# Kernel tuning notes

Hardware: AMD Instinct MI355X
Metric: run time of the kernel (lower is better)

The kernel has to match this reference:

```python
import jax, jax.numpy as jnp
import numpy as np

EPS = 1e-6
NEG = -10000.0
B, T, V, D, H, L, F = 2, 1024, 32000, 1024, 16, 4, 2730
DH = D // H
SCALE = 1.0 / np.sqrt(DH)


def alibi_slopes(n_head):
    # standard ALiBi geometric slopes (n_head is a power of 2 here)
    start = 2.0 ** (-8.0 / n_head)
    return jnp.asarray([start ** (i + 1) for i in range(n_head)], dtype=jnp.float32)


def rational_softmax(x, eps=EPS):
    # exp-free softmax: Pade [0/2] rational surrogate of exp on shifted (<=0) scores
    s = x - jnp.max(x, axis=-1, keepdims=True)
    num = 1.0 / (1.0 - s + 0.5 * s * s)
    return num / (jnp.sum(num, axis=-1, keepdims=True) + eps)


def me_norm(x, w, eps=EPS):
    # mean-error norm: x / (mean|x| + eps) * w
    return x / (jnp.mean(jnp.abs(x), axis=-1, keepdims=True) + eps) * w


def setup_inputs() -> dict:
    key = jax.random.key(0)
    ks = jax.random.split(key, 9)
    std = 0.02
    return {
        "input_ids": jax.random.randint(ks[0], (B, T), 0, V),
        "embed_w":   jax.random.normal(ks[1], (V, D), jnp.float32) * std,  # tied with head
        "qkv_w":     jax.random.normal(ks[2], (L, 3 * D, D), jnp.float32) * std,
        "out_w":     jax.random.normal(ks[3], (L, D, D), jnp.float32) * std,
        "gate_w":    jax.random.normal(ks[4], (L, 2 * F, D), jnp.float32) * std,
        "wout_w":    jax.random.normal(ks[5], (L, D, F), jnp.float32) * std,
        "norm1_w":   jnp.ones((L, D), jnp.float32),
        "norm2_w":   jnp.ones((L, D), jnp.float32),
        "normf_w":   jnp.ones((D,), jnp.float32),
    }


def _forward(input_ids, embed_w, qkv_w, out_w, gate_w, wout_w, norm1_w, norm2_w, normf_w):
    slopes = alibi_slopes(H)                       # [H]
    pos = jnp.arange(T)
    rel = jnp.abs(pos[:, None] - pos[None, :]).astype(jnp.float32)  # [T,T]
    alibi = -rel[None] * slopes[:, None, None]     # [H,T,T]
    causal = jnp.triu(jnp.ones((T, T), bool), k=1) # future positions

    x = embed_w[input_ids]                         # [B,T,D]

    def block(x, p):
        w_qkv, w_out, w_gate, w_wout, n1, n2 = p
        h = me_norm(x, n1)
        qkv = (h @ w_qkv.T).reshape(B, T, 3, H, DH).transpose(2, 0, 3, 1, 4)
        q, k, v = qkv[0], qkv[1], qkv[2]           # [B,H,T,DH]
        scores = jnp.einsum('bhtd,bhsd->bhts', q, k) * SCALE + alibi
        scores = jnp.where(causal[None, None], NEG, scores)
        probs = rational_softmax(scores)
        o = jnp.einsum('bhts,bhsd->bhtd', probs, v)
        o = o.transpose(0, 2, 1, 3).reshape(B, T, D)
        x = x + o @ w_out.T
        h = me_norm(x, n2)
        gv = h @ w_gate.T                           # [B,T,2F]
        gate, val = gv[..., :F], gv[..., F:]
        sigma = 0.5 * (gate / (jnp.abs(gate) + 1.0) + 1.0)  # rational sigmoid
        x = x + (gate * sigma * val) @ w_wout.T
        return x, None

    x, _ = jax.lax.scan(block, x, (qkv_w, out_w, gate_w, wout_w, norm1_w, norm2_w))
    x = me_norm(x, normf_w)
    logits = x @ embed_w.T                          # tied head, [B,T,V]
    return logits


def reference(input_ids, embed_w, qkv_w, out_w, gate_w, wout_w, norm1_w, norm2_w, normf_w):
    return _forward(input_ids, embed_w, qkv_w, out_w, gate_w, wout_w, norm1_w, norm2_w, normf_w)
```

## Files before the change

### kernel.cpp

```cpp
#include <hip/hip_runtime.h>
#include <math.h>

typedef __attribute__((ext_vector_type(8))) short bf16x8;
typedef __attribute__((ext_vector_type(4))) float f32x4;

namespace {
constexpr int Bc = 2, Tc = 1024, Dc = 1024, Hc = 16, Fc = 2730;
constexpr int Fp = 2752;
constexpr int Gp = 5504;
constexpr int Mc = Bc * Tc;
constexpr float EPSc = 1e-6f;
constexpr float NEGc = -10000.0f;
constexpr float SCALEc = 0.125f;
}

__device__ __forceinline__ unsigned short f2b(float f) {
    unsigned int u = __float_as_uint(f);
    u += 0x7FFFu + ((u >> 16) & 1u);
    return (unsigned short)(u >> 16);
}

__global__ void k_embed(const int* __restrict__ ids, const float* __restrict__ ew,
                        float* __restrict__ x) {
    int row = blockIdx.x;
    int id = ids[row];
    const float4* src = (const float4*)(ew + (size_t)id * Dc);
    float4* dst = (float4*)(x + (size_t)row * Dc);
    dst[threadIdx.x] = src[threadIdx.x];
}

__global__ void k_conv(const float* __restrict__ in, unsigned short* __restrict__ out) {
    size_t i = ((size_t)blockIdx.x * 256 + threadIdx.x) * 4;
    float4 v = *(const float4*)(in + i);
    ushort4 o;
    o.x = f2b(v.x); o.y = f2b(v.y); o.z = f2b(v.z); o.w = f2b(v.w);
    *(ushort4*)(out + i) = o;
}

__global__ void k_conv_gate_ilv(const float* __restrict__ in, unsigned short* __restrict__ out) {
    int r = blockIdx.x;
    int c = threadIdx.x * 4;
    ushort4 o;
    if (r < 2 * Fc) {
        int src = (r >> 1) + (r & 1) * Fc;
        float4 v = *(const float4*)(in + (size_t)src * Dc + c);
        o.x = f2b(v.x); o.y = f2b(v.y); o.z = f2b(v.z); o.w = f2b(v.w);
    } else {
        o.x = o.y = o.z = o.w = 0;
    }
    *(ushort4*)(out + (size_t)r * Dc + c) = o;
}

__global__ void k_conv_padk(const float* __restrict__ in, unsigned short* __restrict__ out) {
    int r = blockIdx.x;
    for (int c = threadIdx.x; c < Fp; c += 256) {
        float v = (c < Fc) ? in[(size_t)r * Fc + c] : 0.0f;
        out[(size_t)r * Fp + c] = f2b(v);
    }
}

__global__ void k_menorm_b(const float* __restrict__ x, const float* __restrict__ w,
                           unsigned short* __restrict__ out) {
    int row = blockIdx.x;
    float4 v = ((const float4*)(x + (size_t)row * Dc))[threadIdx.x];
    float s = fabsf(v.x) + fabsf(v.y) + fabsf(v.z) + fabsf(v.w);
#pragma unroll
    for (int m = 32; m >= 1; m >>= 1) s += __shfl_xor(s, m);
    __shared__ float ws4[4];
    if ((threadIdx.x & 63) == 0) ws4[threadIdx.x >> 6] = s;
    __syncthreads();
    float tot = ws4[0] + ws4[1] + ws4[2] + ws4[3];
    float inv = 1.0f / (tot / (float)Dc + EPSc);
    float4 wv = ((const float4*)w)[threadIdx.x];
    ushort4 o;
    o.x = f2b(v.x * inv * wv.x);
    o.y = f2b(v.y * inv * wv.y);
    o.z = f2b(v.z * inv * wv.z);
    o.w = f2b(v.w * inv * wv.w);
    ((ushort4*)(out + (size_t)row * Dc))[threadIdx.x] = o;
}

template <int MODE, int BM>
__global__ __launch_bounds__(256) void k_mfma_gemm(
    const unsigned short* __restrict__ A, const unsigned short* __restrict__ Bw,
    const float* __restrict__ Res, float* __restrict__ C,
    unsigned short* __restrict__ U0, unsigned short* __restrict__ U1,
    unsigned short* __restrict__ U2, int N, int K) {
    constexpr int MFR = BM / 32;
    __shared__ __align__(16) unsigned short As[BM * 64];
    __shared__ __align__(16) unsigned short Bs[128 * 64];
    const int tid = threadIdx.x;
    const int lane = tid & 63;
    const int wid = tid >> 6;
    const int wr = wid >> 1, wc = wid & 1;
    const int l15 = lane & 15, g = lane >> 4;

    const int nwg = gridDim.x * gridDim.y;
    int w = blockIdx.y * gridDim.x + blockIdx.x;
    int f = (nwg & 7) ? w : ((w & 7) * (nwg >> 3) + (w >> 3));
    const int bm = (f % gridDim.x) * BM, bn = (f / gridDim.x) * 128;

    f32x4 acc[MFR][4] = {};

    const int nk = K >> 6;
    for (int kt = 0; kt < nk; ++kt) {
        const int k0 = kt << 6;
#pragma unroll
        for (int it = 0; it < MFR; ++it) {
            int ci = it * 256 + tid;
            int r = ci >> 3;
            int sc = (ci & 7) ^ (r & 7);
            __builtin_amdgcn_global_load_lds(
                (const __attribute__((address_space(1))) void*)(A + (size_t)(bm + r) * K + k0 + sc * 8),
                (__attribute__((address_space(3))) void*)(As + ci * 8), 16, 0, 0);
        }
#pragma unroll
        for (int it = 0; it < 4; ++it) {
            int ci = it * 256 + tid;
            int r = ci >> 3;
            int sc = (ci & 7) ^ (r & 7);
            __builtin_amdgcn_global_load_lds(
                (const __attribute__((address_space(1))) void*)(Bw + (size_t)(bn + r) * K + k0 + sc * 8),
                (__attribute__((address_space(3))) void*)(Bs + ci * 8), 16, 0, 0);
        }
        __syncthreads();
#pragma unroll
        for (int kk = 0; kk < 2; ++kk) {
            bf16x8 af[MFR], bfr[4];
            const int kc = kk * 4 + g;
#pragma unroll
            for (int m = 0; m < MFR; ++m) {
                int row = wr * (BM / 2) + m * 16 + l15;
                af[m] = *(const bf16x8*)&As[(row * 8 + (kc ^ (row & 7))) * 8];
            }
#pragma unroll
            for (int n = 0; n < 4; ++n) {
                int col = wc * 64 + n * 16 + l15;
                bfr[n] = *(const bf16x8*)&Bs[(col * 8 + (kc ^ (col & 7))) * 8];
            }
#pragma unroll
            for (int m = 0; m < MFR; ++m)
#pragma unroll
                for (int n = 0; n < 4; ++n)
                    acc[m][n] = __builtin_amdgcn_mfma_f32_16x16x32_bf16(af[m], bfr[n], acc[m][n], 0, 0, 0);
        }
        __syncthreads();
    }

#pragma unroll
    for (int m = 0; m < MFR; ++m) {
        int row0 = bm + wr * (BM / 2) + m * 16 + (g << 2);
#pragma unroll
        for (int n = 0; n < 4; ++n) {
            int col = bn + wc * 64 + n * 16 + l15;
            if constexpr (MODE == 0 || MODE == 1) {
#pragma unroll
                for (int j = 0; j < 4; ++j) {
                    size_t idx = (size_t)(row0 + j) * N + col;
                    float v = acc[m][n][j];
                    if (MODE == 1) v += Res[idx];
                    C[idx] = v;
                }
            } else if constexpr (MODE == 2) {
                if (col < 2048) {
                    unsigned short* dst = (col < 1024) ? U0 : U1;
                    int hh = (col & 1023) >> 6, dh = col & 63;
#pragma unroll
                    for (int j = 0; j < 4; ++j) {
                        int row = row0 + j;
                        int b = row >> 10, t = row & 1023;
                        dst[((size_t)((b * Hc + hh) * Tc + t)) * 64 + dh] = f2b(acc[m][n][j]);
                    }
                } else {
                    int hh = (col >> 6) & 15, dh = col & 63;
                    int b = row0 >> 10, t = row0 & 1023;
                    ushort4 o4;
                    o4.x = f2b(acc[m][n][0]); o4.y = f2b(acc[m][n][1]);
                    o4.z = f2b(acc[m][n][2]); o4.w = f2b(acc[m][n][3]);
                    *(ushort4*)&U2[((size_t)((b * Hc + hh) * 64 + dh)) * Tc + t] = o4;
                }
            } else {
                float pv[4];
#pragma unroll
                for (int j = 0; j < 4; ++j) pv[j] = __shfl_xor(acc[m][n][j], 1);
                if ((l15 & 1) == 0) {
                    int fq = col >> 1;
#pragma unroll
                    for (int j = 0; j < 4; ++j) {
                        float gate = acc[m][n][j], val = pv[j];
                        float sigma = 0.5f * (gate / (fabsf(gate) + 1.0f) + 1.0f);
                        U0[(size_t)(row0 + j) * Fp + fq] = f2b(gate * sigma * val);
                    }
                }
            }
        }
    }
}

__global__ __launch_bounds__(256) void k_attn_mfma(
    const unsigned short* __restrict__ Qh, const unsigned short* __restrict__ Kh,
    const unsigned short* __restrict__ Vt, unsigned short* __restrict__ o) {
    const int q0 = blockIdx.x * 64;
    const int h = blockIdx.y, b = blockIdx.z;
    const int bh = b * Hc + h;
    const float slope = exp2f(-0.5f * (float)(h + 1));

    __shared__ __align__(16) unsigned short Ks[64 * 64];
    __shared__ __align__(16) unsigned short Vs[64 * 64];
    __shared__ __align__(16) unsigned short Ps[4][16 * 64];

    const int tid = threadIdx.x, lane = tid & 63, wid = tid >> 6;
    const int q0w = q0 + wid * 16;
    const int l15 = lane & 15, g = lane >> 4;

    const unsigned short* qbase = Qh + ((size_t)(bh * Tc + q0w + l15)) * 64 + g * 8;
    bf16x8 qf[2];
    qf[0] = *(const bf16x8*)qbase;
    qf[1] = *(const bf16x8*)(qbase + 32);

    const int nt = q0 / 64 + 1;

    f32x4 mx = {-3e38f, -3e38f, -3e38f, -3e38f};
    for (int it = 0; it < nt; ++it) {
        const int st = it * 64;
        __syncthreads();
#pragma unroll
        for (int half = 0; half < 2; ++half) {
            int ci = half * 256 + tid;
            int r = ci >> 3, sc = (ci & 7) ^ (r & 7);
            __builtin_amdgcn_global_load_lds(
                (const __attribute__((address_space(1))) void*)(Kh + ((size_t)(bh * Tc + st + r)) * 64 + sc * 8),
                (__attribute__((address_space(3))) void*)(Ks + ci * 8), 16, 0, 0);
        }
        __syncthreads();
#pragma unroll
        for (int si = 0; si < 4; ++si) {
            f32x4 d = {0.f, 0.f, 0.f, 0.f};
#pragma unroll
            for (int kc = 0; kc < 2; ++kc) {
                int r2 = si * 16 + l15;
                int c2 = kc * 4 + g;
                bf16x8 bk = *(const bf16x8*)&Ks[(r2 * 8 + (c2 ^ (r2 & 7))) * 8];
                d = __builtin_amdgcn_mfma_f32_16x16x32_bf16(qf[kc], bk, d, 0, 0, 0);
            }
            int s = st + si * 16 + l15;
#pragma unroll
            for (int j = 0; j < 4; ++j) {
                int t = q0w + g * 4 + j;
                float scv = (s <= t) ? d[j] * SCALEc - slope * (float)(t - s) : -3e38f;
                mx[j] = fmaxf(mx[j], scv);
            }
        }
    }
#pragma unroll
    for (int m = 8; m >= 1; m >>= 1)
#pragma unroll
        for (int j = 0; j < 4; ++j) mx[j] = fmaxf(mx[j], __shfl_xor(mx[j], m));

    f32x4 sum = {0.f, 0.f, 0.f, 0.f};
    f32x4 oacc[4] = {};
    for (int it = 0; it < nt; ++it) {
        const int st = it * 64;
        __syncthreads();
#pragma unroll
        for (int half = 0; half < 2; ++half) {
            int ci = half * 256 + tid;
            int r = ci >> 3, sc = (ci & 7) ^ (r & 7);
            __builtin_amdgcn_global_load_lds(
                (const __attribute__((address_space(1))) void*)(Kh + ((size_t)(bh * Tc + st + r)) * 64 + sc * 8),
                (__attribute__((address_space(3))) void*)(Ks + ci * 8), 16, 0, 0);
            __builtin_amdgcn_global_load_lds(
                (const __attribute__((address_space(1))) void*)(Vt + ((size_t)(bh * 64 + r)) * Tc + st + sc * 8),
                (__attribute__((address_space(3))) void*)(Vs + ci * 8), 16, 0, 0);
        }
        __syncthreads();
#pragma unroll
        for (int si = 0; si < 4; ++si) {
            f32x4 d = {0.f, 0.f, 0.f, 0.f};
#pragma unroll
            for (int kc = 0; kc < 2; ++kc) {
                int r2 = si * 16 + l15;
                int c2 = kc * 4 + g;
                bf16x8 bk = *(const bf16x8*)&Ks[(r2 * 8 + (c2 ^ (r2 & 7))) * 8];
                d = __builtin_amdgcn_mfma_f32_16x16x32_bf16(qf[kc], bk, d, 0, 0, 0);
            }
            int sl = si * 16 + l15;
            int s = st + sl;
            int chunk = sl >> 3, coff = sl & 7;
#pragma unroll
            for (int j = 0; j < 4; ++j) {
                int t = q0w + g * 4 + j;
                int q = g * 4 + j;
                unsigned short pb = 0;
                if (s <= t) {
                    float sv = d[j] * SCALEc - slope * (float)(t - s) - mx[j];
                    float num = __builtin_amdgcn_rcpf(fmaf(0.5f * sv, sv, 1.0f - sv));
                    sum[j] += num;
                    pb = f2b(num);
                }
                Ps[wid][q * 64 + ((chunk ^ (q & 7)) * 8) + coff] = pb;
            }
        }
        __syncthreads();
#pragma unroll
        for (int kc = 0; kc < 2; ++kc) {
            int c2 = kc * 4 + g;
            bf16x8 pa = *(const bf16x8*)&Ps[wid][(l15 * 8 + (c2 ^ (l15 & 7))) * 8];
#pragma unroll
            for (int n = 0; n < 4; ++n) {
                int r2 = n * 16 + l15;
                bf16x8 vb = *(const bf16x8*)&Vs[(r2 * 8 + (c2 ^ (r2 & 7))) * 8];
                oacc[n] = __builtin_amdgcn_mfma_f32_16x16x32_bf16(pa, vb, oacc[n], 0, 0, 0);
            }
        }
    }
#pragma unroll
    for (int m = 8; m >= 1; m >>= 1)
#pragma unroll
        for (int j = 0; j < 4; ++j) sum[j] += __shfl_xor(sum[j], m);

#pragma unroll
    for (int j = 0; j < 4; ++j) {
        int t = q0w + g * 4 + j;
        float svm = NEGc - mx[j];
        float mnum = __builtin_amdgcn_rcpf(fmaf(0.5f * svm, svm, 1.0f - svm));
        float inv = __builtin_amdgcn_rcpf(sum[j] + (float)(Tc - 1 - t) * mnum + EPSc);
#pragma unroll
        for (int n = 0; n < 4; ++n) {
            o[((size_t)(b * Tc + t)) * Dc + h * 64 + n * 16 + l15] = f2b(oacc[n][j] * inv);
        }
    }
}

extern "C" void kernel_launch(void* const* d_in, const int* in_sizes, int n_in,
                              void* d_out, int out_size, void* d_ws, size_t ws_size,
                              hipStream_t stream) {
    const int* ids = (const int*)d_in[0];
    const float* embed_w = (const float*)d_in[1];
    const float* qkv_w = (const float*)d_in[2];
    const float* out_w = (const float*)d_in[3];
    const float* gate_w = (const float*)d_in[4];
    const float* wout_w = (const float*)d_in[5];
    const float* n1 = (const float*)d_in[6];
    const float* n2 = (const float*)d_in[7];
    const float* nf = (const float*)d_in[8];
    float* outp = (float*)d_out;

    char* ws = (char*)d_ws;
    float* x = (float*)(ws + 0);
    unsigned short* h = (unsigned short*)(ws + 8388608);
    unsigned short* Qh = (unsigned short*)(ws + 12582912);
    unsigned short* Kh = (unsigned short*)(ws + 16777216);
    unsigned short* Vt = (unsigned short*)(ws + 20971520);
    unsigned short* g = (unsigned short*)(ws + 25165824);
    unsigned short* w1 = (unsigned short*)(ws + 36438016);
    unsigned short* wo_b = (unsigned short*)(ws + 42729472);
    unsigned short* wg_b = (unsigned short*)(ws + 44826624);
    unsigned short* emb_b = (unsigned short*)(ws + 12582912);

    dim3 blk(256);

    k_embed<<<dim3(Mc), blk, 0, stream>>>(ids, embed_w, x);

    for (int l = 0; l < 4; l++) {
        const float* wq = qkv_w + (size_t)l * 3 * Dc * Dc;
        const float* wo = out_w + (size_t)l * Dc * Dc;
        const float* wg = gate_w + (size_t)l * 2 * Fc * Dc;
        const float* ww = wout_w + (size_t)l * Dc * Fc;

        k_conv<<<dim3(3072), blk, 0, stream>>>(wq, w1);
        k_conv<<<dim3(1024), blk, 0, stream>>>(wo, wo_b);
        k_conv_gate_ilv<<<dim3(Gp), blk, 0, stream>>>(wg, wg_b);

        k_menorm_b<<<dim3(Mc), blk, 0, stream>>>(x, n1 + (size_t)l * Dc, h);
        k_mfma_gemm<2, 128><<<dim3(16, 24), blk, 0, stream>>>(h, w1, nullptr, nullptr, Qh, Kh, Vt, 3 * Dc, Dc);
        k_conv_padk<<<dim3(1024), blk, 0, stream>>>(ww, w1);
        k_attn_mfma<<<dim3(Tc / 64, Hc, Bc), blk, 0, stream>>>(Qh, Kh, Vt, h);
        k_mfma_gemm<1, 64><<<dim3(32, 8), blk, 0, stream>>>(h, wo_b, x, x, nullptr, nullptr, nullptr, Dc, Dc);
        k_menorm_b<<<dim3(Mc), blk, 0, stream>>>(x, n2 + (size_t)l * Dc, h);
        k_mfma_gemm<3, 128><<<dim3(16, Gp / 128), blk, 0, stream>>>(h, wg_b, nullptr, nullptr, g, nullptr, nullptr, Gp, Dc);
        k_mfma_gemm<1, 64><<<dim3(32, 8), blk, 0, stream>>>(g, w1, x, x, nullptr, nullptr, nullptr, Dc, Fp);
    }

    k_menorm_b<<<dim3(Mc), blk, 0, stream>>>(x, nf, h);
    k_conv<<<dim3(32000), blk, 0, stream>>>(embed_w, emb_b);
    k_mfma_gemm<0, 128><<<dim3(16, 250), blk, 0, stream>>>(h, emb_b, nullptr, outp, nullptr, nullptr, nullptr, 32000, Dc);
}
```

Before: 1.053 ms.

## Add 256x256 eight-wave pipelined GEMM for the tied LM head

Adds a 512-thread GEMM kernel for the final vocabulary projection. It uses 256x256 tiles, double-buffered direct global-to-LDS loads with an XOR swizzle, XCD-aware block remapping, and MFMA phases raised with s_setprio. It replaces the 128-tile generic GEMM for the largest matmul to get more reuse per loaded tile and to overlap loads with MFMA work. The cost is a large LDS footprint (128KB) and 128 accumulators per thread, which may limit occupancy. The grid is only 1000 blocks.

```diff
diff --git a/kernel.cpp b/kernel.cpp
--- a/kernel.cpp
+++ b/kernel.cpp
@@ -197,6 +197,114 @@
     }
 }
 
+__global__ __launch_bounds__(512, 2) void k_gemm_8ph(
+    const unsigned short* __restrict__ A, const unsigned short* __restrict__ Bw,
+    float* __restrict__ C, int N, int K) {
+    __shared__ __align__(16) unsigned short As[2][256 * 64];
+    __shared__ __align__(16) unsigned short Bs[2][256 * 64];
+    const int tid = threadIdx.x;
+    const int lane = tid & 63, wid = tid >> 6;
+    const int wm = wid >> 2, wn = wid & 3;
+    const int l15 = lane & 15, g = lane >> 4;
+
+    const int nwg = gridDim.x * gridDim.y;
+    int w = blockIdx.y * gridDim.x + blockIdx.x;
+    int f = (nwg & 7) ? w : ((w & 7) * (nwg >> 3) + (w >> 3));
+    const int bm = (f % gridDim.x) * 256;
+    const int bn = (f / gridDim.x) * 256;
+
+    const int nk = K >> 6;
+
+    f32x4 acc[8][4] = {};
+
+#define STAGE8(buf, kt)                                                                          \
+    {                                                                                            \
+        _Pragma("unroll") for (int it = 0; it < 4; ++it) {                                       \
+            int ci = it * 512 + tid;                                                             \
+            int r = ci >> 3, c = (ci & 7) ^ (r & 7);                                             \
+            __builtin_amdgcn_global_load_lds(                                                    \
+                (const __attribute__((address_space(1))) void*)(A + (size_t)(bm + r) * K + (kt) * 64 + c * 8), \
+                (__attribute__((address_space(3))) void*)(&As[buf][ci * 8]), 16, 0, 0);          \
+        }                                                                                        \
+        _Pragma("unroll") for (int it = 0; it < 4; ++it) {                                       \
+            int ci = it * 512 + tid;                                                             \
+            int r = ci >> 3, c = (ci & 7) ^ (r & 7);                                             \
+            __builtin_amdgcn_global_load_lds(                                                    \
+                (const __attribute__((address_space(1))) void*)(Bw + (size_t)(bn + r) * K + (kt) * 64 + c * 8), \
+                (__attribute__((address_space(3))) void*)(&Bs[buf][ci * 8]), 16, 0, 0);          \
+        }                                                                                        \
+    }
+
+    STAGE8(0, 0);
+    STAGE8(1, 1);
+    asm volatile("s_waitcnt vmcnt(8)" ::: "memory");
+    __builtin_amdgcn_s_barrier();
+
+    for (int kt = 0; kt < nk; ++kt) {
+        const int buf = kt & 1;
+        const unsigned short* Ab = As[buf];
+        const unsigned short* Bb = Bs[buf];
+        bf16x8 bfr[4][2];
+#pragma unroll
+        for (int p = 0; p < 4; ++p) {
+            bf16x8 af[2][2];
+#pragma unroll
+            for (int le = 0; le < 2; ++le) {
+                int row = wm * 128 + (p * 2 + le) * 16 + l15;
+#pragma unroll
+                for (int kk = 0; kk < 2; ++kk) {
+                    int kc = kk * 4 + g;
+                    af[le][kk] = *(const bf16x8*)&Ab[(row * 8 + (kc ^ (row & 7))) * 8];
+                }
+            }
+            if (p == 0) {
+#pragma unroll
+                for (int n = 0; n < 4; ++n) {
+                    int col = wn * 64 + n * 16 + l15;
+#pragma unroll
+                    for (int kk = 0; kk < 2; ++kk) {
+                        int kc = kk * 4 + g;
+                        bfr[n][kk] = *(const bf16x8*)&Bb[(col * 8 + (kc ^ (col & 7))) * 8];
+                    }
+                }
+            }
+            __builtin_amdgcn_s_barrier();
+            if (p == 3 && kt + 2 < nk) STAGE8(buf, kt + 2);
+            __builtin_amdgcn_s_setprio(1);
+#pragma unroll
+            for (int kk = 0; kk < 2; ++kk)
+#pragma unroll
+                for (int le = 0; le < 2; ++le)
+#pragma unroll
+                    for (int n = 0; n < 4; ++n)
+                        acc[p * 2 + le][n] = __builtin_amdgcn_mfma_f32_16x16x32_bf16(
+                            af[le][kk], bfr[n][kk], acc[p * 2 + le][n], 0, 0, 0);
+            __builtin_amdgcn_s_setprio(0);
+            if (p == 3) {
+                if (kt + 2 < nk) {
+                    asm volatile("s_waitcnt vmcnt(8)" ::: "memory");
+                } else {
+                    asm volatile("s_waitcnt vmcnt(0)" ::: "memory");
+                }
+            }
+            __builtin_amdgcn_s_barrier();
+        }
+    }
+#undef STAGE8
+
+#pragma unroll
+    for (int m = 0; m < 8; ++m) {
+        int row0 = bm + wm * 128 + m * 16 + (g << 2);
+#pragma unroll
+        for (int n = 0; n < 4; ++n) {
+            int col = bn + wn * 64 + n * 16 + l15;
+#pragma unroll
+            for (int j = 0; j < 4; ++j)
+                C[(size_t)(row0 + j) * N + col] = acc[m][n][j];
+        }
+    }
+}
+
 __global__ __launch_bounds__(256) void k_attn_mfma(
     const unsigned short* __restrict__ Qh, const unsigned short* __restrict__ Kh,
     const unsigned short* __restrict__ Vt, unsigned short* __restrict__ o) {
@@ -384,5 +492,5 @@
 
     k_menorm_b<<<dim3(Mc), blk, 0, stream>>>(x, nf, h);
     k_conv<<<dim3(32000), blk, 0, stream>>>(embed_w, emb_b);
-    k_mfma_gemm<0, 128><<<dim3(16, 250), blk, 0, stream>>>(h, emb_b, nullptr, outp, nullptr, nullptr, nullptr, 32000, Dc);
-}
+    k_gemm_8ph<<<dim3(8, 125), dim3(512), 0, stream>>>(h, emb_b, outp, 32000, Dc);
+}
```

Result: faster. 1.027 ms (-2.4%).
